# Kernel optimization log

Hardware: AMD Instinct MI355X
Metric: run time of the kernel (lower is better)

## Reference

```python
import jax, jax.numpy as jnp
import numpy as np

INF = 100000000.0
TOPK = 27


def _box_iou(a, b):
    # a: [N,4] (x1,y1,x2,y2), b: [G,4] -> iou [N,G]
    area_a = (a[:, 2] - a[:, 0]) * (a[:, 3] - a[:, 1])
    area_b = (b[:, 2] - b[:, 0]) * (b[:, 3] - b[:, 1])
    lt = jnp.maximum(a[:, None, :2], b[None, :, :2])
    rb = jnp.minimum(a[:, None, 2:], b[None, :, 2:])
    wh = jnp.clip(rb - lt, 0.0)
    inter = wh[..., 0] * wh[..., 1]
    union = area_a[:, None] + area_b[None, :] - inter
    return inter / union, union


def _assign_one(anchors, gts, tokens):
    # anchors [N,4], gts [G,4], tokens [G,T]
    N = anchors.shape[0]
    G = gts.shape[0]
    ious, _ = _box_iou(anchors, gts)  # [N,G]

    a_cx = (anchors[:, 2] + anchors[:, 0]) * 0.5
    a_cy = (anchors[:, 3] + anchors[:, 1]) * 0.5
    g_cx = (gts[:, 2] + gts[:, 0]) * 0.5
    g_cy = (gts[:, 3] + gts[:, 1]) * 0.5

    # pairwise center distance [N,G]
    dist = jnp.sqrt((a_cx[:, None] - g_cx[None, :]) ** 2 +
                    (a_cy[:, None] - g_cy[None, :]) ** 2)

    # topk nearest anchors per gt (smallest distance) -> idxs [G,TOPK]
    _, topk_idxs = jax.lax.top_k(-dist.T, TOPK)

    # candidate ious [G,TOPK]
    cand = jnp.take_along_axis(ious.T, topk_idxs, axis=1)
    iou_mean = cand.mean(axis=1)
    iou_std = cand.std(axis=1, ddof=1)  # torch.std is unbiased
    is_pos = cand >= (iou_mean + iou_std)[:, None]

    # center-inside-gt check [G,TOPK]
    ax = a_cx[topk_idxs]
    ay = a_cy[topk_idxs]
    l = ax - gts[:, 0:1]
    t = ay - gts[:, 1:2]
    r = gts[:, 2:3] - ax
    b = gts[:, 3:4] - ay
    is_in_gts = jnp.minimum(jnp.minimum(l, t), jnp.minimum(r, b)) > 0.01
    is_pos = is_pos & is_in_gts

    # scatter candidate ious into flat [G*N] buffer of -INF (indices are unique)
    flat_idx = (jnp.arange(G)[:, None] * N + topk_idxs).reshape(-1)
    vals = ious.T.reshape(-1)[flat_idx]
    scat = jnp.where(is_pos.reshape(-1), vals, -INF)
    ious_inf = jnp.full((G * N,), -INF, dtype=ious.dtype).at[flat_idx].set(scat)
    ious_inf = ious_inf.reshape(G, N).T  # [N,G]

    anchors_to_gt_values = ious_inf.max(axis=1)          # [N]
    anchors_to_gt_indexs = ious_inf.argmax(axis=1)       # [N]

    matched_gts = gts[anchors_to_gt_indexs]              # [N,4]

    T = tokens.shape[1]
    unmatched = jnp.zeros((T,), tokens.dtype).at[-1].set(1.0)
    token_labels = jnp.where((anchors_to_gt_values == -INF)[:, None],
                             unmatched[None, :],
                             tokens[anchors_to_gt_indexs])  # [N,T]
    return anchors_to_gt_values, anchors_to_gt_indexs, matched_gts, token_labels


def setup_inputs() -> dict:
    key = jax.random.key(0)
    k1, k2, k3, k4, k5 = jax.random.split(key, 5)
    B, N, G, T = 8, 100000, 64, 256
    # anchors: valid x1<x2, y1<y2 boxes on a ~1024px canvas
    a_c = jax.random.uniform(k1, (B, N, 2), jnp.float32, 0.0, 1024.0)
    a_wh = jax.random.uniform(k2, (B, N, 2), jnp.float32, 8.0, 128.0)
    anchor_boxes = jnp.concatenate([a_c - a_wh / 2, a_c + a_wh / 2], axis=-1)
    g_c = jax.random.uniform(k3, (B, G, 2), jnp.float32, 0.0, 1024.0)
    g_wh = jax.random.uniform(k4, (B, G, 2), jnp.float32, 64.0, 512.0)
    gt_boxes = jnp.concatenate([g_c - g_wh / 2, g_c + g_wh / 2], axis=-1)
    token_map = jax.random.uniform(k5, (B, G, T), jnp.float32)
    return {"anchor_boxes": anchor_boxes, "gt_boxes": gt_boxes,
            "token_map": token_map}


def reference(anchor_boxes, gt_boxes, token_map):
    return jax.vmap(_assign_one)(anchor_boxes, gt_boxes, token_map)
```

## Files before the change

kernel.cpp:

```cpp
#include <hip/hip_runtime.h>
#include <cstdint>

constexpr int B = 8, N = 100000, G = 64, T = 256, TOPK = 27;
constexpr int BN = B * N;
constexpr int CAP = 2048;
#define NEG_INF_VAL (-100000000.0f)

typedef float v4f __attribute__((ext_vector_type(4)));

__global__ __launch_bounds__(256) void atss_centers_kernel(
    const float* __restrict__ anchors, float2* __restrict__ ctr,
    unsigned long long* __restrict__ best)
{
#pragma clang fp contract(off)
  int i = blockIdx.x * 256 + threadIdx.x;
  if (i < BN) {
    float4 ab = ((const float4*)anchors)[i];
    ctr[i] = make_float2((ab.z + ab.x) * 0.5f, (ab.w + ab.y) * 0.5f);
    best[i] = 0ULL;
  }
}

__global__ __launch_bounds__(1024) void atss_assign_kernel(
    const float* __restrict__ anchors,
    const float2* __restrict__ ctr,
    const float* __restrict__ gts,
    unsigned long long* __restrict__ best)
{
#pragma clang fp contract(off)
  __shared__ float s_d[CAP];
  __shared__ int   s_i[CAP];
  __shared__ int   s_cnt;
  __shared__ int   s_sel[TOPK];
  __shared__ float s_iou[TOPK];
  __shared__ int   s_in[TOPK];
  __shared__ float s_thresh;

  const int bid = blockIdx.x;
  const int bg  = (bid & 7) * (B * G / 8) + (bid >> 3);
  const int b   = bg / G;
  const int g   = bg % G;
  const int tid = threadIdx.x;

  const float4 gbox = ((const float4*)gts)[bg];
  const float g_cx = (gbox.z + gbox.x) * 0.5f;
  const float g_cy = (gbox.w + gbox.y) * 0.5f;

  const float4*  abase = (const float4*)(anchors + (size_t)b * N * 4);
  const float2*  cbase = ctr + (size_t)b * N;
  const float4*  c4    = (const float4*)cbase;

  float thr2 = 24.0f * 24.0f;
  int M = 0;
  for (int attempt = 0; attempt < 8; ++attempt) {
    if (tid == 0) s_cnt = 0;
    __syncthreads();
    for (int m = tid; m < N / 4; m += 1024) {
      float4 ca = c4[2 * m];
      float4 cb = c4[2 * m + 1];
      float dx0 = ca.x - g_cx, dy0 = ca.y - g_cy;
      float d20 = __fmul_rn(dx0, dx0) + __fmul_rn(dy0, dy0);
      float dx1 = ca.z - g_cx, dy1 = ca.w - g_cy;
      float d21 = __fmul_rn(dx1, dx1) + __fmul_rn(dy1, dy1);
      float dx2 = cb.x - g_cx, dy2 = cb.y - g_cy;
      float d22 = __fmul_rn(dx2, dx2) + __fmul_rn(dy2, dy2);
      float dx3 = cb.z - g_cx, dy3 = cb.w - g_cy;
      float d23 = __fmul_rn(dx3, dx3) + __fmul_rn(dy3, dy3);
      if (d20 < thr2) {
        int p = atomicAdd(&s_cnt, 1);
        if (p < CAP) { s_d[p] = __fsqrt_rn(d20); s_i[p] = 4 * m; }
      }
      if (d21 < thr2) {
        int p = atomicAdd(&s_cnt, 1);
        if (p < CAP) { s_d[p] = __fsqrt_rn(d21); s_i[p] = 4 * m + 1; }
      }
      if (d22 < thr2) {
        int p = atomicAdd(&s_cnt, 1);
        if (p < CAP) { s_d[p] = __fsqrt_rn(d22); s_i[p] = 4 * m + 2; }
      }
      if (d23 < thr2) {
        int p = atomicAdd(&s_cnt, 1);
        if (p < CAP) { s_d[p] = __fsqrt_rn(d23); s_i[p] = 4 * m + 3; }
      }
    }
    __syncthreads();
    int cnt = s_cnt;
    __syncthreads();
    if (cnt >= TOPK && cnt <= CAP) { M = cnt; break; }
    thr2 = (cnt < TOPK) ? thr2 * 16.0f : thr2 * 0.25f;
  }

  for (int s = tid; s < M; s += 1024) {
    unsigned long long pk_s =
        ((unsigned long long)__float_as_uint(s_d[s]) << 20) |
        (unsigned long long)(unsigned)s_i[s];
    int rank = 0;
    for (int j = 0; j < M; ++j) {
      unsigned long long pk_j =
          ((unsigned long long)__float_as_uint(s_d[j]) << 20) |
          (unsigned long long)(unsigned)s_i[j];
      rank += (pk_j < pk_s) ? 1 : 0;
    }
    if (rank < TOPK) s_sel[rank] = s_i[s];
  }
  __syncthreads();

  if (tid < TOPK) {
    int a = s_sel[tid];
    float4 ab = abase[a];
    float area_a = __fmul_rn(ab.z - ab.x, ab.w - ab.y);
    float area_b = __fmul_rn(gbox.z - gbox.x, gbox.w - gbox.y);
    float ltx = fmaxf(ab.x, gbox.x), lty = fmaxf(ab.y, gbox.y);
    float rbx = fminf(ab.z, gbox.z), rby = fminf(ab.w, gbox.w);
    float w = fmaxf(rbx - ltx, 0.0f), h = fmaxf(rby - lty, 0.0f);
    float inter = __fmul_rn(w, h);
    float uni = (area_a + area_b) - inter;
    s_iou[tid] = inter / uni;
    float acx = (ab.z + ab.x) * 0.5f, acy = (ab.w + ab.y) * 0.5f;
    float l = acx - gbox.x, t = acy - gbox.y;
    float r = gbox.z - acx, bt = gbox.w - acy;
    float mn = fminf(fminf(l, t), fminf(r, bt));
    s_in[tid] = (mn > 0.01f) ? 1 : 0;
  }
  __syncthreads();

  if (tid == 0) {
    float sum = 0.0f;
    for (int k = 0; k < TOPK; ++k) sum += s_iou[k];
    float mean = sum / (float)TOPK;
    float vs = 0.0f;
    for (int k = 0; k < TOPK; ++k) {
      float d = s_iou[k] - mean;
      vs += __fmul_rn(d, d);
    }
    float sd = __fsqrt_rn(vs / (float)(TOPK - 1));
    s_thresh = mean + sd;
  }
  __syncthreads();

  if (tid < TOPK) {
    float iou = s_iou[tid];
    if (s_in[tid] && iou >= s_thresh) {
      unsigned long long pk =
          ((unsigned long long)__float_as_uint(iou) << 32) |
          (unsigned long long)(0xFFFFFFFFu - (unsigned)g);
      atomicMax(&best[(size_t)b * N + s_sel[tid]], pk);
    }
  }
}

__global__ __launch_bounds__(256) void atss_write_kernel(
    const unsigned long long* __restrict__ best,
    const float* __restrict__ gts,
    const float* __restrict__ tokens,
    float* __restrict__ out)
{
  float* __restrict__ out_val = out;
  float* __restrict__ out_idx = out + (size_t)BN;
  float* __restrict__ out_mg  = out + (size_t)2 * BN;
  float* __restrict__ out_tok = out + (size_t)6 * BN;

  __shared__ int s_row[256];

  const int tid = threadIdx.x;
  const int i0  = blockIdx.x * 256;
  const int i   = i0 + tid;

  unsigned long long p = best[i];
  const int b_ = i / N;
  int g = 0;
  float val = NEG_INF_VAL;
  if (p != 0ULL) {
    g   = (int)(0xFFFFFFFFu - (unsigned)(p & 0xFFFFFFFFULL));
    val = __uint_as_float((unsigned)(p >> 32));
  }
  const int row = b_ * G + g;
  s_row[tid] = (p != 0ULL) ? row : -1;

  out_val[i] = val;
  out_idx[i] = (float)g;
  ((v4f*)out_mg)[i] = ((const v4f*)gts)[row];
  __syncthreads();

  const int lane = tid & 63;
  const int sub  = tid >> 6;
  const v4f* tok4 = (const v4f*)tokens;
#pragma unroll 8
  for (int s = 0; s < 64; ++s) {
    int a = (s << 2) + sub;
    int r = s_row[a];
    v4f t;
    if (r >= 0) {
      t = tok4[(size_t)r * 64 + lane];
    } else {
      t = (v4f){0.0f, 0.0f, 0.0f, 0.0f};
      if (lane == 63) t.w = 1.0f;
    }
    ((v4f*)(out_tok + (size_t)(i0 + a) * T))[lane] = t;
  }
}

extern "C" void kernel_launch(void* const* d_in, const int* in_sizes, int n_in,
                              void* d_out, int out_size, void* d_ws, size_t ws_size,
                              hipStream_t stream) {
  const float* anchors = (const float*)d_in[0];
  const float* gts     = (const float*)d_in[1];
  const float* tokens  = (const float*)d_in[2];
  float* out = (float*)d_out;

  unsigned long long* best = (unsigned long long*)d_ws;
  float2* ctr = (float2*)((char*)d_ws + sizeof(unsigned long long) * (size_t)BN);

  atss_centers_kernel<<<BN / 256, 256, 0, stream>>>(anchors, ctr, best);
  atss_assign_kernel<<<B * G, 1024, 0, stream>>>(anchors, ctr, gts, best);
  atss_write_kernel<<<BN / 256, 256, 0, stream>>>(best, gts, tokens, out);
}
```

Baseline: 846.7 us.

## Split token write into persistent grid-stride kernel with prefetched best entries

Splits the final write kernel in two: a scalar kernel writes the value, index and matched-box outputs, and a separate token kernel writes the 256-float token rows. The token kernel runs a fixed grid of 2048 blocks in which each wavefront handles one row per iteration, striding across all rows and prefetching the next row's best entry. This is meant to reduce launch and tail overhead on the dominant ~800 MB token write and to hide the latency of the best lookup. It adds one kernel launch and reads the best array twice.

```diff
diff --git a/kernel.cpp b/kernel.cpp
--- a/kernel.cpp
+++ b/kernel.cpp
@@ -4,6 +4,7 @@
 constexpr int B = 8, N = 100000, G = 64, T = 256, TOPK = 27;
 constexpr int BN = B * N;
 constexpr int CAP = 2048;
+constexpr int TOKEN_BLOCKS = 2048;
 #define NEG_INF_VAL (-100000000.0f)
 
 typedef float v4f __attribute__((ext_vector_type(4)));
@@ -149,23 +150,16 @@
   }
 }
 
-__global__ __launch_bounds__(256) void atss_write_kernel(
+__global__ __launch_bounds__(256) void atss_scalar_write_kernel(
     const unsigned long long* __restrict__ best,
     const float* __restrict__ gts,
-    const float* __restrict__ tokens,
     float* __restrict__ out)
 {
   float* __restrict__ out_val = out;
   float* __restrict__ out_idx = out + (size_t)BN;
   float* __restrict__ out_mg  = out + (size_t)2 * BN;
-  float* __restrict__ out_tok = out + (size_t)6 * BN;
-
-  __shared__ int s_row[256];
-
-  const int tid = threadIdx.x;
-  const int i0  = blockIdx.x * 256;
-  const int i   = i0 + tid;
-
+
+  const int i = blockIdx.x * 256 + threadIdx.x;
   unsigned long long p = best[i];
   const int b_ = i / N;
   int g = 0;
@@ -175,28 +169,39 @@
     val = __uint_as_float((unsigned)(p >> 32));
   }
   const int row = b_ * G + g;
-  s_row[tid] = (p != 0ULL) ? row : -1;
-
   out_val[i] = val;
   out_idx[i] = (float)g;
   ((v4f*)out_mg)[i] = ((const v4f*)gts)[row];
-  __syncthreads();
-
-  const int lane = tid & 63;
-  const int sub  = tid >> 6;
+}
+
+__global__ __launch_bounds__(256) void atss_token_kernel(
+    const unsigned long long* __restrict__ best,
+    const float* __restrict__ tokens,
+    float* __restrict__ out)
+{
+  float* __restrict__ out_tok = out + (size_t)6 * BN;
+  const int lane = threadIdx.x & 63;
+  const int NW   = TOKEN_BLOCKS * 4;
+  int row = (blockIdx.x << 2) | (threadIdx.x >> 6);
   const v4f* tok4 = (const v4f*)tokens;
-#pragma unroll 8
-  for (int s = 0; s < 64; ++s) {
-    int a = (s << 2) + sub;
-    int r = s_row[a];
+
+  unsigned long long p = best[row];
+  while (true) {
+    const int nrow = row + NW;
+    unsigned long long pn = (nrow < BN) ? best[nrow] : 0ULL;
     v4f t;
-    if (r >= 0) {
-      t = tok4[(size_t)r * 64 + lane];
+    if (p != 0ULL) {
+      const int b_ = row / N;
+      const int g  = (int)(0xFFFFFFFFu - (unsigned)(p & 0xFFFFFFFFULL));
+      t = tok4[(size_t)(b_ * G + g) * 64 + lane];
     } else {
       t = (v4f){0.0f, 0.0f, 0.0f, 0.0f};
       if (lane == 63) t.w = 1.0f;
     }
-    ((v4f*)(out_tok + (size_t)(i0 + a) * T))[lane] = t;
+    ((v4f*)(out_tok + (size_t)row * T))[lane] = t;
+    if (nrow >= BN) break;
+    row = nrow;
+    p = pn;
   }
 }
 
@@ -213,5 +218,6 @@
 
   atss_centers_kernel<<<BN / 256, 256, 0, stream>>>(anchors, ctr, best);
   atss_assign_kernel<<<B * G, 1024, 0, stream>>>(anchors, ctr, gts, best);
-  atss_write_kernel<<<BN / 256, 256, 0, stream>>>(best, gts, tokens, out);
-}
+  atss_scalar_write_kernel<<<BN / 256, 256, 0, stream>>>(best, gts, out);
+  atss_token_kernel<<<TOKEN_BLOCKS, 256, 0, stream>>>(best, tokens, out);
+}
```

New measurement: 846.5 us. Within noise of the previous version (-0.0%).
